# Kernel optimization log

Measured on AMD Instinct MI355X. Metric: run time of the kernel, lower is better.

The kernel has to match this reference:

```python
import jax, jax.numpy as jnp
import numpy as np

N = 20000      # nodes
IN = 256       # in_dim
OUT = 128      # out_dim
S = 8          # num_sect
K = S + 1      # sectors + self branch
EP = 40000     # edges per sector


def setup_inputs() -> dict:
    key = jax.random.key(0)
    ks = jax.random.split(key, 10)
    x = jax.random.normal(ks[0], (N, IN), jnp.float32)
    rows = jax.random.randint(ks[1], (S, EP), 0, N)  # src (adj row)
    cols = jax.random.randint(ks[2], (S, EP), 0, N)  # dst (adj col)
    # degree norms (buffers derived from the graph, as in compute_norm)
    out_deg = np.bincount(np.asarray(rows).ravel(), minlength=N).astype(np.float32)
    in_deg = np.bincount(np.asarray(cols).ravel(), minlength=N).astype(np.float32)
    out_norm = jnp.asarray(np.clip(out_deg, 1.0, None) ** -0.5)[:, None]  # [N,1]
    in_norm = jnp.asarray(np.clip(in_deg, 1.0, None) ** -0.5)[:, None]    # [N,1]
    s = 0.05  # xavier-ish scale
    W_self = jax.random.normal(ks[3], (IN, OUT), jnp.float32) * s
    W_sect = jax.random.normal(ks[4], (S, IN, OUT), jnp.float32) * s
    WC = jax.random.normal(ks[5], (OUT, OUT), jnp.float32) * s
    WD = jax.random.normal(ks[6], (OUT, OUT), jnp.float32) * s
    gate_w = jax.random.normal(ks[7], (2 * K * OUT, 1), jnp.float32) * s
    gate_b = jnp.zeros((1,), jnp.float32)
    return {"x": x, "W_self": W_self, "W_sect": W_sect, "WC": WC, "WD": WD,
            "gate_w": gate_w, "gate_b": gate_b, "out_norm": out_norm,
            "in_norm": in_norm, "rows": rows, "cols": cols}


def reference(x, W_self, W_sect, WC, WD, gate_w, gate_b, out_norm, in_norm, rows, cols):
    n = x.shape[0]
    # --- forward_sector_agg (dropout is identity in eval / drop_rate=0) ---
    z_self = x @ W_self                                    # [N, OUT]
    H = jnp.einsum('ni,sio->sno', x, W_sect) * out_norm    # [S, N, OUT]
    def agg(h, r, c):  # sparse adj @ h : z[src] += h[dst]
        return jax.ops.segment_sum(h[c], r, num_segments=n)
    Z = jax.vmap(agg)(H, rows, cols)                       # [S, N, OUT]
    z = jnp.concatenate([z_self[None], Z], axis=0)         # [K, N, OUT]
    z = jnp.transpose(z, (1, 0, 2)) * in_norm[:, :, None]  # [N, K, OUT]
    # --- heter_sen_interaction ---
    zc = z @ WC                                            # [N, K, D]
    com = jnp.einsum('nkd,njd->nkj', zc, zc)
    ac = jax.nn.softmax(com, axis=2)
    z_com = jnp.einsum('nkj,njd->nkd', ac, zc).reshape(n, -1)
    zd = z @ WD
    sub = zd[:, :, None, :] - zd[:, None, :, :]            # [N, K, K, D]
    ds = jnp.einsum('nkd,nkjd->nkj', zd, sub)
    ad = jax.nn.softmax(ds, axis=2)
    z_dis = jnp.einsum('nkj,nkjd->nkd', ad, sub).reshape(n, -1)
    cat = jnp.concatenate([z_com, z_dis], axis=-1)         # [N, 2*K*D]
    beta = jax.nn.sigmoid(cat @ gate_w + gate_b)           # [N, 1]
    return beta * z_com + (1.0 - beta) * z_dis             # [N, K*D]
```

## Files before the change

### kernel.cpp

```cpp
#include <hip/hip_runtime.h>
#include <math.h>

#define N_NODES 20000
#define IN_DIM  256
#define OUT_DIM 128
#define S_SECT  8
#define K_BR    9
#define NK      (K_BR*OUT_DIM)
#define EP_EDGE 40000
#define N_EDGES (S_SECT*EP_EDGE)
#define N_BINS  (S_SECT*N_NODES)
#define SCAN_BLOCKS 160
#define M_ROWS  (N_NODES*K_BR)
#define ZP      136
#define TP      136

typedef float v4f __attribute__((ext_vector_type(4)));
typedef short v8s __attribute__((ext_vector_type(8)));

__device__ inline unsigned short f2bf(float f) {
  union { float f; unsigned u; } v; v.f = f;
  unsigned r = v.u + 0x7fff + ((v.u >> 16) & 1);
  return (unsigned short)(r >> 16);
}
__device__ inline float bf2f(unsigned short h) {
  union { unsigned u; float f; } v; v.u = ((unsigned)h) << 16;
  return v.f;
}

__global__ __launch_bounds__(256) void k_prep(
    const float* __restrict__ Wself, const float* __restrict__ Wsect,
    const float* __restrict__ WC, const float* __restrict__ WD,
    unsigned short* __restrict__ Wtg, unsigned short* __restrict__ Btg)
{
  const int id = blockIdx.x * 256 + threadIdx.x;
  if (id < NK*IN_DIM) {
    const int j = id >> 8, k = id & 255;
    float w;
    if (j < OUT_DIM) w = Wself[(size_t)k*OUT_DIM + j];
    else {
      const int s = (j - OUT_DIM) >> 7, c = (j - OUT_DIM) & 127;
      w = Wsect[(size_t)s*(IN_DIM*OUT_DIM) + (size_t)k*OUT_DIM + c];
    }
    Wtg[id] = f2bf(w);
  } else {
    const int id2 = id - NK*IN_DIM;
    if (id2 < 256*128) {
      const int n = id2 >> 7, k = id2 & 127;
      const float w = (n < OUT_DIM) ? WC[k*OUT_DIM + n] : WD[k*OUT_DIM + (n - OUT_DIM)];
      Btg[id2] = f2bf(w);
    }
  }
}

__global__ __launch_bounds__(256, 4) void k_gemm_xw_mfma(
    const float* __restrict__ x, const unsigned short* __restrict__ Wtg,
    const float* __restrict__ outn, const float* __restrict__ inn,
    unsigned short* __restrict__ Hbuf, unsigned short* __restrict__ Zbufh)
{
  __shared__ unsigned short Bls[128*ZP];
  const int t = threadIdx.x;
  const int wave = t >> 6, lane = t & 63;
  const int mrow = lane & 15, quad = lane >> 4;
  const int m0 = blockIdx.x * 64 + wave * 16;

  v8s afr[8];
  {
    const int r = m0 + mrow;
    const bool ok = (r < N_NODES);
    const float* src = x + (size_t)r*IN_DIM + quad*8;
    #pragma unroll
    for (int kq = 0; kq < 8; ++kq) {
      float4 a0 = {0.f,0.f,0.f,0.f}, a1 = {0.f,0.f,0.f,0.f};
      if (ok) {
        a0 = *(const float4*)(src + kq*32);
        a1 = *(const float4*)(src + kq*32 + 4);
      }
      v8s f;
      f[0] = (short)f2bf(a0.x); f[1] = (short)f2bf(a0.y);
      f[2] = (short)f2bf(a0.z); f[3] = (short)f2bf(a0.w);
      f[4] = (short)f2bf(a1.x); f[5] = (short)f2bf(a1.y);
      f[6] = (short)f2bf(a1.z); f[7] = (short)f2bf(a1.w);
      afr[kq] = f;
    }
  }

  for (int jj = 0; jj < 3; ++jj) {
    const int jb = blockIdx.y * 3 + jj;

    v4f acc[8];
    #pragma unroll
    for (int jt = 0; jt < 8; ++jt) acc[jt] = (v4f){0.f,0.f,0.f,0.f};

    for (int kh = 0; kh < 2; ++kh) {
      #pragma unroll
      for (int i = 0; i < 8; ++i) {
        const int idx = t + i*256;
        const int row = idx >> 4, c8 = idx & 15;
        *(uint4*)(Bls + row*ZP + c8*8) =
            *(const uint4*)(Wtg + (size_t)(jb*128 + row)*IN_DIM + kh*128 + c8*8);
      }
      __syncthreads();

      #pragma unroll
      for (int kq = 0; kq < 4; ++kq) {
        #pragma unroll
        for (int jt = 0; jt < 8; ++jt) {
          const v8s bf = *(const v8s*)(Bls + (jt*16 + mrow)*ZP + kq*32 + quad*8);
          acc[jt] = __builtin_amdgcn_mfma_f32_16x16x32_bf16(afr[kh*4 + kq], bf, acc[jt], 0, 0, 0);
        }
      }
      __syncthreads();
    }

    if (jb == 0) {
      #pragma unroll
      for (int p = 0; p < 4; ++p) {
        const int R = m0 + quad*4 + p;
        if (R >= N_NODES) continue;
        const float iw = inn[R];
        #pragma unroll
        for (int jt = 0; jt < 8; ++jt)
          Zbufh[(size_t)R*NK + jt*16 + mrow] = f2bf(acc[jt][p] * iw);
      }
    } else {
      const int s = jb - 1;
      #pragma unroll
      for (int p = 0; p < 4; ++p) {
        const int R = m0 + quad*4 + p;
        if (R >= N_NODES) continue;
        const float ow = outn[R];
        #pragma unroll
        for (int jt = 0; jt < 8; ++jt)
          Hbuf[((size_t)s*N_NODES + R)*OUT_DIM + jt*16 + mrow] = f2bf(acc[jt][p] * ow);
      }
    }
  }
}

__global__ __launch_bounds__(256) void k_count(
    const int* __restrict__ rows, int* __restrict__ cnt)
{
  const int id = blockIdx.x * 256 + threadIdx.x;
  if (id >= N_EDGES) return;
  const int s = id / EP_EDGE;
  atomicAdd(&cnt[s * N_NODES + rows[id]], 1);
}

__global__ __launch_bounds__(256) void k_scan1(
    const int* __restrict__ cnt, int* __restrict__ bsum)
{
  __shared__ int sh[256];
  const int t = threadIdx.x;
  const int base = blockIdx.x * 1000;
  int s = 0;
  if (t < 250) {
    const int i = base + t*4;
    s = cnt[i] + cnt[i+1] + cnt[i+2] + cnt[i+3];
  }
  sh[t] = s; __syncthreads();
  for (int off = 128; off > 0; off >>= 1) {
    if (t < off) sh[t] += sh[t + off];
    __syncthreads();
  }
  if (t == 0) bsum[blockIdx.x] = sh[0];
}

__global__ void k_scan2(const int* __restrict__ bsum, int* __restrict__ boff)
{
  if (threadIdx.x == 0) {
    int acc = 0;
    for (int b = 0; b < SCAN_BLOCKS; ++b) { boff[b] = acc; acc += bsum[b]; }
  }
}

__global__ __launch_bounds__(256) void k_scan3(
    const int* __restrict__ cnt, const int* __restrict__ boff,
    int* __restrict__ offs)
{
  __shared__ int sh[256];
  const int t = threadIdx.x;
  const int base = blockIdx.x * 1000;
  int v[4] = {0,0,0,0};
  int mySum = 0;
  if (t < 250) {
    const int i = base + t*4;
    v[0]=cnt[i]; v[1]=cnt[i+1]; v[2]=cnt[i+2]; v[3]=cnt[i+3];
    mySum = v[0]+v[1]+v[2]+v[3];
  }
  sh[t] = mySum; __syncthreads();
  for (int off = 1; off < 256; off <<= 1) {
    int add = (t >= off) ? sh[t - off] : 0;
    __syncthreads();
    sh[t] += add;
    __syncthreads();
  }
  if (t < 250) {
    int excl = boff[blockIdx.x] + sh[t] - mySum;
    const int i = base + t*4;
    offs[i]   = excl;           excl += v[0];
    offs[i+1] = excl;           excl += v[1];
    offs[i+2] = excl;           excl += v[2];
    offs[i+3] = excl;
  }
}

__global__ __launch_bounds__(256) void k_scatter(
    const int* __restrict__ rows, const int* __restrict__ cols,
    const int* __restrict__ offs, int* __restrict__ cur,
    int* __restrict__ eCol)
{
  const int id = blockIdx.x * 256 + threadIdx.x;
  if (id >= N_EDGES) return;
  const int s = id / EP_EDGE;
  const int bin = s * N_NODES + rows[id];
  const int pos = offs[bin] + atomicAdd(&cur[bin], 1);
  eCol[pos] = cols[id];
}

__global__ __launch_bounds__(256) void k_agg_csr(
    const unsigned short* __restrict__ Hbuf, const int* __restrict__ offs,
    const int* __restrict__ cnt, const int* __restrict__ eCol,
    const float* __restrict__ inn, unsigned short* __restrict__ Zbufh)
{
  const long long tid = (long long)blockIdx.x * 256 + threadIdx.x;
  const int group = (int)(tid >> 5);
  if (group >= N_BINS) return;
  const int lane = (int)(tid & 31);
  const int s = group / N_NODES;
  const int r = group - s * N_NODES;
  const int start = offs[group];
  const int n = cnt[group];
  float4 acc = {0.f, 0.f, 0.f, 0.f};
  for (int i = 0; i < n; ++i) {
    const int c = eCol[start + i];
    const uint2 h = *(const uint2*)(Hbuf + ((size_t)s*N_NODES + c)*OUT_DIM + lane*4);
    acc.x += bf2f((unsigned short)h.x);
    acc.y += bf2f((unsigned short)(h.x >> 16));
    acc.z += bf2f((unsigned short)h.y);
    acc.w += bf2f((unsigned short)(h.y >> 16));
  }
  const float w = inn[r];
  uint2 o;
  o.x = (unsigned)f2bf(acc.x * w) | ((unsigned)f2bf(acc.y * w) << 16);
  o.y = (unsigned)f2bf(acc.z * w) | ((unsigned)f2bf(acc.w * w) << 16);
  *(uint2*)(Zbufh + ((size_t)r*K_BR + 1 + s)*OUT_DIM + lane*4) = o;
}

__global__ __launch_bounds__(512, 4) void k_zcd_interact(
    const unsigned short* __restrict__ Zbufh, const unsigned short* __restrict__ Btg,
    const float* __restrict__ gw, const float* __restrict__ gb,
    float* __restrict__ out)
{
  __shared__ unsigned short Bls[64*ZP];
  __shared__ unsigned short tls[8][2][9*TP];
  __shared__ float graw[8][2][K_BR][10];
  __shared__ float gs[8][2][K_BR][10];
  const int t = threadIdx.x;
  const int wv = t >> 6, lane = t & 63;
  const int mrow = lane & 15, quad = lane >> 4;
  const int n0 = blockIdx.x * 8;
  const int rowbase = (n0 + wv)*9;

  v8s afr[4];
  {
    const bool ok = (mrow < 9);
    const unsigned short* src = Zbufh + (size_t)(rowbase + mrow)*OUT_DIM + quad*8;
    #pragma unroll
    for (int kq = 0; kq < 4; ++kq) {
      v8s f = {0,0,0,0,0,0,0,0};
      if (ok) f = *(const v8s*)(src + kq*32);
      afr[kq] = f;
    }
  }

  for (int jh = 0; jh < 2; ++jh) {
    v4f acc[8];
    #pragma unroll
    for (int j = 0; j < 8; ++j) acc[j] = (v4f){0.f,0.f,0.f,0.f};

    for (int sub = 0; sub < 2; ++sub) {
      #pragma unroll
      for (int i = 0; i < 2; ++i) {
        const int idx = t + i*512;
        const int row = idx >> 4, c8 = idx & 15;
        *(uint4*)(Bls + row*ZP + c8*8) =
            *(const uint4*)(Btg + (size_t)(jh*128 + sub*64 + row)*OUT_DIM + c8*8);
      }
      __syncthreads();
      #pragma unroll
      for (int jl = 0; jl < 4; ++jl) {
        const unsigned short* bp = Bls + (jl*16 + mrow)*ZP + quad*8;
        #pragma unroll
        for (int kq = 0; kq < 4; ++kq) {
          const v8s bf = *(const v8s*)(bp + kq*32);
          acc[sub*4+jl] = __builtin_amdgcn_mfma_f32_16x16x32_bf16(bf, afr[kq], acc[sub*4+jl], 0, 0, 0);
        }
      }
      __syncthreads();
    }

    if (mrow < 9) {
      unsigned short* dst = &tls[wv][jh][mrow*TP];
      #pragma unroll
      for (int a = 0; a < 8; ++a) {
        const int off = (a >> 2)*64 + (a & 3)*16 + quad*4;
        uint2 o;
        o.x = (unsigned)f2bf(acc[a][0]) | ((unsigned)f2bf(acc[a][1]) << 16);
        o.y = (unsigned)f2bf(acc[a][2]) | ((unsigned)f2bf(acc[a][3]) << 16);
        *(uint2*)(dst + off) = o;
      }
    }
  }

  {
    const int r = lane & 15;
    #pragma unroll
    for (int mat = 0; mat < 2; ++mat) {
      const unsigned short* src = &tls[wv][mat][r*TP + quad*8];
      v8s frag[4];
      #pragma unroll
      for (int kq = 0; kq < 4; ++kq) {
        v8s f = {0,0,0,0,0,0,0,0};
        if (r < K_BR) f = *(const v8s*)(src + kq*32);
        frag[kq] = f;
      }
      v4f acc = {0.f,0.f,0.f,0.f};
      #pragma unroll
      for (int kq = 0; kq < 4; ++kq)
        acc = __builtin_amdgcn_mfma_f32_16x16x32_bf16(frag[kq], frag[kq], acc, 0, 0, 0);
      if (r < K_BR) {
        #pragma unroll
        for (int p = 0; p < 4; ++p) {
          const int m = quad*4 + p;
          if (m < K_BR) graw[wv][mat][m][r] = acc[p];
        }
      }
    }
  }

  if (lane < 18) {
    const int mat = (lane >= 9) ? 1 : 0;
    const int k   = lane - mat*9;
    float v[9];
    if (mat == 0) {
      #pragma unroll
      for (int j = 0; j < 9; ++j) v[j] = graw[wv][0][k][j];
    } else {
      const float gkk = graw[wv][1][k][k];
      #pragma unroll
      for (int j = 0; j < 9; ++j) v[j] = gkk - graw[wv][1][k][j];
    }
    float m = v[0];
    #pragma unroll
    for (int j = 1; j < 9; ++j) m = fmaxf(m, v[j]);
    float sum = 0.f;
    #pragma unroll
    for (int j = 0; j < 9; ++j) { v[j] = expf(v[j] - m); sum += v[j]; }
    const float inv = 1.f / sum;
    #pragma unroll
    for (int j = 0; j < 9; ++j) gs[wv][mat][k][j] = v[j] * inv;
  }

  const float gbv = gb[0];
  float gwc[2][9], gwd[2][9];
  #pragma unroll
  for (int dd = 0; dd < 2; ++dd) {
    const int d = lane + dd*64;
    #pragma unroll
    for (int j = 0; j < 9; ++j) {
      gwc[dd][j] = gw[j*OUT_DIM + d];
      gwd[dd][j] = gw[NK + j*OUT_DIM + d];
    }
  }

  float zcj[2][9], zdj[2][9];
  #pragma unroll
  for (int dd = 0; dd < 2; ++dd) {
    const int d = lane + dd*64;
    #pragma unroll
    for (int j = 0; j < 9; ++j) {
      zcj[dd][j] = bf2f(tls[wv][0][j*TP + d]);
      zdj[dd][j] = bf2f(tls[wv][1][j*TP + d]);
    }
  }
  float zcomK[2][9], zdisK[2][9];
  float gp = 0.f;
  #pragma unroll
  for (int k = 0; k < 9; ++k) {
    #pragma unroll
    for (int dd = 0; dd < 2; ++dd) {
      float zc = 0.f, ad = 0.f;
      #pragma unroll
      for (int j = 0; j < 9; ++j) {
        zc += gs[wv][0][k][j] * zcj[dd][j];
        ad += gs[wv][1][k][j] * zdj[dd][j];
      }
      zcomK[dd][k] = zc;
      zdisK[dd][k] = zdj[dd][k] - ad;
      gp += zc * gwc[dd][k] + zdisK[dd][k] * gwd[dd][k];
    }
  }
  #pragma unroll
  for (int off = 32; off > 0; off >>= 1) gp += __shfl_xor(gp, off, 64);
  const float beta = 1.f / (1.f + expf(-(gp + gbv)));
  #pragma unroll
  for (int k = 0; k < 9; ++k) {
    #pragma unroll
    for (int dd = 0; dd < 2; ++dd) {
      const int d = lane + dd*64;
      out[(size_t)(n0+wv)*NK + k*OUT_DIM + d] =
          beta*zcomK[dd][k] + (1.f-beta)*zdisK[dd][k];
    }
  }
}

extern "C" void kernel_launch(void* const* d_in, const int* in_sizes, int n_in,
                              void* d_out, int out_size, void* d_ws, size_t ws_size,
                              hipStream_t stream)
{
  const float* x     = (const float*)d_in[0];
  const float* Wself = (const float*)d_in[1];
  const float* Wsect = (const float*)d_in[2];
  const float* WC    = (const float*)d_in[3];
  const float* WD    = (const float*)d_in[4];
  const float* gw    = (const float*)d_in[5];
  const float* gb    = (const float*)d_in[6];
  const float* outn  = (const float*)d_in[7];
  const float* inn   = (const float*)d_in[8];
  const int*   rows  = (const int*)d_in[9];
  const int*   cols  = (const int*)d_in[10];
  float* out = (float*)d_out;

  char* p = (char*)d_ws;
  unsigned short* Hbuf  = (unsigned short*)p; p += (size_t)S_SECT*N_NODES*OUT_DIM*2;
  unsigned short* Zbufh = (unsigned short*)p; p += (size_t)M_ROWS*OUT_DIM*2;
  int* cnt    = (int*)p;                      p += (size_t)N_BINS*4;
  int* offs   = (int*)p;                      p += (size_t)N_BINS*4;
  int* cur    = (int*)p;                      p += (size_t)N_BINS*4;
  int* bsum   = (int*)p;                      p += 256*4;
  int* boff   = (int*)p;                      p += 256*4;
  int* eCol   = (int*)p;                      p += (size_t)N_EDGES*4;
  unsigned short* Btg = (unsigned short*)p;   p += 256*128*2;
  unsigned short* Wtg = (unsigned short*)p;   p += (size_t)NK*IN_DIM*2;

  hipMemsetAsync(cnt, 0, (size_t)N_BINS*4, stream);
  hipMemsetAsync(cur, 0, (size_t)N_BINS*4, stream);

  k_prep<<<(NK*IN_DIM + 256*128 + 255)/256, 256, 0, stream>>>(Wself, Wsect, WC, WD, Wtg, Btg);

  dim3 gA((N_NODES + 63)/64, 3);
  k_gemm_xw_mfma<<<gA, 256, 0, stream>>>(x, Wtg, outn, inn, Hbuf, Zbufh);

  const int eb = (N_EDGES + 255)/256;
  k_count  <<<eb, 256, 0, stream>>>(rows, cnt);
  k_scan1  <<<SCAN_BLOCKS, 256, 0, stream>>>(cnt, bsum);
  k_scan2  <<<1, 64, 0, stream>>>(bsum, boff);
  k_scan3  <<<SCAN_BLOCKS, 256, 0, stream>>>(cnt, boff, offs);
  k_scatter<<<eb, 256, 0, stream>>>(rows, cols, offs, cur, eCol);

  const int aggBlocks = (N_BINS*32 + 255)/256;
  k_agg_csr<<<aggBlocks, 256, 0, stream>>>(Hbuf, offs, cnt, eCol, inn, Zbufh);

  k_zcd_interact<<<N_NODES/8, 512, 0, stream>>>(Zbufh, Btg, gw, gb, out);
}
```

Baseline: 292.0 us.

## Shrink LDS footprint and raise occupancy in interaction kernel with packed float math

Measured after the change: 301.1 us. 1.03x slower.

```diff
diff --git a/kernel.cpp b/kernel.cpp
--- a/kernel.cpp
+++ b/kernel.cpp
@@ -16,6 +16,7 @@
 #define TP      136
 
 typedef float v4f __attribute__((ext_vector_type(4)));
+typedef float v2f __attribute__((ext_vector_type(2)));
 typedef short v8s __attribute__((ext_vector_type(8)));
 
 __device__ inline unsigned short f2bf(float f) {
@@ -247,15 +248,14 @@
   *(uint2*)(Zbufh + ((size_t)r*K_BR + 1 + s)*OUT_DIM + lane*4) = o;
 }
 
-__global__ __launch_bounds__(512, 4) void k_zcd_interact(
+__global__ __launch_bounds__(512, 6) void k_zcd_interact(
     const unsigned short* __restrict__ Zbufh, const unsigned short* __restrict__ Btg,
     const float* __restrict__ gw, const float* __restrict__ gb,
     float* __restrict__ out)
 {
-  __shared__ unsigned short Bls[64*ZP];
+  __shared__ unsigned short Bls[32*ZP];
   __shared__ unsigned short tls[8][2][9*TP];
-  __shared__ float graw[8][2][K_BR][10];
-  __shared__ float gs[8][2][K_BR][10];
+  __shared__ float gg[8][2][K_BR][10];
   const int t = threadIdx.x;
   const int wv = t >> 6, lane = t & 63;
   const int mrow = lane & 15, quad = lane >> 4;
@@ -279,22 +279,20 @@
     #pragma unroll
     for (int j = 0; j < 8; ++j) acc[j] = (v4f){0.f,0.f,0.f,0.f};
 
-    for (int sub = 0; sub < 2; ++sub) {
-      #pragma unroll
-      for (int i = 0; i < 2; ++i) {
-        const int idx = t + i*512;
-        const int row = idx >> 4, c8 = idx & 15;
+    for (int st = 0; st < 4; ++st) {
+      {
+        const int row = t >> 4, c8 = t & 15;
         *(uint4*)(Bls + row*ZP + c8*8) =
-            *(const uint4*)(Btg + (size_t)(jh*128 + sub*64 + row)*OUT_DIM + c8*8);
+            *(const uint4*)(Btg + (size_t)(jh*128 + st*32 + row)*OUT_DIM + c8*8);
       }
       __syncthreads();
       #pragma unroll
-      for (int jl = 0; jl < 4; ++jl) {
+      for (int jl = 0; jl < 2; ++jl) {
         const unsigned short* bp = Bls + (jl*16 + mrow)*ZP + quad*8;
         #pragma unroll
         for (int kq = 0; kq < 4; ++kq) {
           const v8s bf = *(const v8s*)(bp + kq*32);
-          acc[sub*4+jl] = __builtin_amdgcn_mfma_f32_16x16x32_bf16(bf, afr[kq], acc[sub*4+jl], 0, 0, 0);
+          acc[st*2+jl] = __builtin_amdgcn_mfma_f32_16x16x32_bf16(bf, afr[kq], acc[st*2+jl], 0, 0, 0);
         }
       }
       __syncthreads();
@@ -304,11 +302,10 @@
       unsigned short* dst = &tls[wv][jh][mrow*TP];
       #pragma unroll
       for (int a = 0; a < 8; ++a) {
-        const int off = (a >> 2)*64 + (a & 3)*16 + quad*4;
         uint2 o;
         o.x = (unsigned)f2bf(acc[a][0]) | ((unsigned)f2bf(acc[a][1]) << 16);
         o.y = (unsigned)f2bf(acc[a][2]) | ((unsigned)f2bf(acc[a][3]) << 16);
-        *(uint2*)(dst + off) = o;
+        *(uint2*)(dst + a*16 + quad*4) = o;
       }
     }
   }
@@ -333,7 +330,7 @@
         #pragma unroll
         for (int p = 0; p < 4; ++p) {
           const int m = quad*4 + p;
-          if (m < K_BR) graw[wv][mat][m][r] = acc[p];
+          if (m < K_BR) gg[wv][mat][m][r] = acc[p];
         }
       }
     }
@@ -345,11 +342,11 @@
     float v[9];
     if (mat == 0) {
       #pragma unroll
-      for (int j = 0; j < 9; ++j) v[j] = graw[wv][0][k][j];
+      for (int j = 0; j < 9; ++j) v[j] = gg[wv][0][k][j];
     } else {
-      const float gkk = graw[wv][1][k][k];
-      #pragma unroll
-      for (int j = 0; j < 9; ++j) v[j] = gkk - graw[wv][1][k][j];
+      const float gkk = gg[wv][1][k][k];
+      #pragma unroll
+      for (int j = 0; j < 9; ++j) v[j] = gkk - gg[wv][1][k][j];
     }
     float m = v[0];
     #pragma unroll
@@ -359,59 +356,45 @@
     for (int j = 0; j < 9; ++j) { v[j] = expf(v[j] - m); sum += v[j]; }
     const float inv = 1.f / sum;
     #pragma unroll
-    for (int j = 0; j < 9; ++j) gs[wv][mat][k][j] = v[j] * inv;
+    for (int j = 0; j < 9; ++j) gg[wv][mat][k][j] = v[j] * inv;
   }
 
   const float gbv = gb[0];
-  float gwc[2][9], gwd[2][9];
+  v2f gwc[9], gwd[9];
   #pragma unroll
-  for (int dd = 0; dd < 2; ++dd) {
-    const int d = lane + dd*64;
-    #pragma unroll
-    for (int j = 0; j < 9; ++j) {
-      gwc[dd][j] = gw[j*OUT_DIM + d];
-      gwd[dd][j] = gw[NK + j*OUT_DIM + d];
-    }
-  }
-
-  float zcj[2][9], zdj[2][9];
+  for (int j = 0; j < 9; ++j) {
+    gwc[j] = (v2f){ gw[j*OUT_DIM + lane],      gw[j*OUT_DIM + lane + 64] };
+    gwd[j] = (v2f){ gw[NK + j*OUT_DIM + lane], gw[NK + j*OUT_DIM + lane + 64] };
+  }
+
+  v2f zcj[9], zdj[9];
   #pragma unroll
-  for (int dd = 0; dd < 2; ++dd) {
-    const int d = lane + dd*64;
-    #pragma unroll
-    for (int j = 0; j < 9; ++j) {
-      zcj[dd][j] = bf2f(tls[wv][0][j*TP + d]);
-      zdj[dd][j] = bf2f(tls[wv][1][j*TP + d]);
-    }
-  }
-  float zcomK[2][9], zdisK[2][9];
-  float gp = 0.f;
+  for (int j = 0; j < 9; ++j) {
+    zcj[j] = (v2f){ bf2f(tls[wv][0][j*TP + lane]), bf2f(tls[wv][0][j*TP + lane + 64]) };
+    zdj[j] = (v2f){ bf2f(tls[wv][1][j*TP + lane]), bf2f(tls[wv][1][j*TP + lane + 64]) };
+  }
+  v2f zcomK[9], zdisK[9];
+  v2f gp2 = (v2f){0.f, 0.f};
   #pragma unroll
   for (int k = 0; k < 9; ++k) {
-    #pragma unroll
-    for (int dd = 0; dd < 2; ++dd) {
-      float zc = 0.f, ad = 0.f;
-      #pragma unroll
-      for (int j = 0; j < 9; ++j) {
-        zc += gs[wv][0][k][j] * zcj[dd][j];
-        ad += gs[wv][1][k][j] * zdj[dd][j];
-      }
-      zcomK[dd][k] = zc;
-      zdisK[dd][k] = zdj[dd][k] - ad;
-      gp += zc * gwc[dd][k] + zdisK[dd][k] * gwd[dd][k];
-    }
-  }
+    v2f zc = (v2f){0.f,0.f}, ad = (v2f){0.f,0.f};
+    #pragma unroll
+    for (int j = 0; j < 9; ++j) {
+      zc += gg[wv][0][k][j] * zcj[j];
+      ad += gg[wv][1][k][j] * zdj[j];
+    }
+    zcomK[k] = zc;
+    zdisK[k] = zdj[k] - ad;
+    gp2 += zc * gwc[k] + zdisK[k] * gwd[k];
+  }
+  float gp = gp2.x + gp2.y;
   #pragma unroll
   for (int off = 32; off > 0; off >>= 1) gp += __shfl_xor(gp, off, 64);
   const float beta = 1.f / (1.f + expf(-(gp + gbv)));
   #pragma unroll
   for (int k = 0; k < 9; ++k) {
-    #pragma unroll
-    for (int dd = 0; dd < 2; ++dd) {
-      const int d = lane + dd*64;
-      out[(size_t)(n0+wv)*NK + k*OUT_DIM + d] =
-          beta*zcomK[dd][k] + (1.f-beta)*zdisK[dd][k];
-    }
+    out[(size_t)(n0+wv)*NK + k*OUT_DIM + lane]      = beta*zcomK[k].x + (1.f-beta)*zdisK[k].x;
+    out[(size_t)(n0+wv)*NK + k*OUT_DIM + lane + 64] = beta*zcomK[k].y + (1.f-beta)*zdisK[k].y;
   }
 }
 
```
